# Kernel tuning notes

Hardware: AMD Instinct MI355X
Metric: run time of the kernel (lower is better)

The kernel has to match this reference:

```python
import jax, jax.numpy as jnp
import numpy as np

B, S, H = 1, 2048, 2048
E, I = 16, 1408
I_SHARED = 5632
TOP_K = 2


def setup_inputs() -> dict:
    key = jax.random.key(0)
    ks = jax.random.split(key, 8)
    scale = 0.02
    return {
        "hidden_states": jax.random.normal(ks[0], (B, S, H), dtype=jnp.float32),
        "router_w": jax.random.normal(ks[1], (H, E), dtype=jnp.float32) * scale,
        "expert_gate_up_w": jax.random.normal(ks[2], (E, H, 2 * I), dtype=jnp.float32) * scale,
        "expert_out_w": jax.random.normal(ks[3], (E, I, H), dtype=jnp.float32) * scale,
        "shared_ffw_gate_w": jax.random.normal(ks[4], (H, I_SHARED), dtype=jnp.float32) * scale,
        "shared_ffw_inter_w": jax.random.normal(ks[5], (H, I_SHARED), dtype=jnp.float32) * scale,
        "shared_ffw_out_w": jax.random.normal(ks[6], (I_SHARED, H), dtype=jnp.float32) * scale,
        "shared_gate_w": jax.random.normal(ks[7], (H, 1), dtype=jnp.float32) * scale,
        "top_k": TOP_K,
    }


def reference(hidden_states, router_w, expert_gate_up_w, expert_out_w,
              shared_ffw_gate_w, shared_ffw_inter_w, shared_ffw_out_w,
              shared_gate_w, top_k):
    b, s, h = hidden_states.shape
    e = router_w.shape[-1]
    x = hidden_states.reshape(-1, h)  # [T, H]

    # --- Router: softmax over experts, top-k, renormalize (norm_top_k_prob=True) ---
    router_logits = x @ router_w                        # [T, E]
    router_probs = jax.nn.softmax(router_logits, -1)
    top_p, top_i = jax.lax.top_k(router_probs, top_k)   # [T, K]
    top_p = top_p / jnp.sum(top_p, axis=-1, keepdims=True)
    # dense routing matrix [E, T] (matches one_hot-sum-transpose in source)
    one_hot = jax.nn.one_hot(top_i, e, dtype=top_p.dtype)  # [T, K, E]
    routing_full = jnp.sum(one_hot * top_p[..., None], axis=1).T  # [E, T]

    # --- Dense per-expert SwiGLU over ALL tokens (as in QwenMoeExperts) ---
    gate_up = jnp.einsum('th,ehm->etm', x, expert_gate_up_w)  # [E, T, 2I]
    gate, up = jnp.split(gate_up, 2, axis=-1)
    hidden = up * jax.nn.silu(gate)                           # [E, T, I]
    expert_out = jnp.einsum('eti,eih->eth', hidden, expert_out_w)  # [E, T, H]
    expert_contribution = jnp.einsum('eth,et->th', expert_out, routing_full)

    # --- Shared expert (SwiGLU MLP) with sigmoid gate ---
    sgate = jax.nn.silu(x @ shared_ffw_gate_w)
    sinter = x @ shared_ffw_inter_w
    shared_out = (sinter * sgate) @ shared_ffw_out_w          # [T, H]
    shared_out = shared_out * jax.nn.sigmoid(x @ shared_gate_w)

    out = (expert_contribution + shared_out).reshape(b, s, h)
    return out, router_logits
```

## Files before the change

### kernel.cpp

```cpp
#include <hip/hip_runtime.h>
#include <math.h>

typedef __attribute__((ext_vector_type(4))) float f32x4;
typedef __attribute__((ext_vector_type(2))) unsigned int u32x2;
typedef __attribute__((ext_vector_type(4))) unsigned int u32x4;
typedef __attribute__((ext_vector_type(8))) unsigned short u16x8;
typedef __attribute__((ext_vector_type(8))) __bf16 bf16x8;
typedef unsigned short ushort_t;

#define H_DIM 2048
#define T_TOK 2048
#define NEXP 16
#define I_DIM 1408
#define I2_DIM 2816
#define IS_DIM 5632
#define MAXROWS 8192

static __device__ __forceinline__ unsigned short f2bf(float f){
  union { float f; unsigned u; } v; v.f = f;
  unsigned r = v.u + 0x7FFFu + ((v.u >> 16) & 1u);
  return (unsigned short)(r >> 16);
}
static __device__ __forceinline__ float bf2f(unsigned short h){
  union { unsigned u; float f; } v; v.u = ((unsigned)h) << 16;
  return v.f;
}
static __device__ __forceinline__ float silu_f(float x){ return x / (1.f + __expf(-x)); }

static __device__ __forceinline__ void gld16(const ushort_t* g, ushort_t* l){
  __builtin_amdgcn_global_load_lds(
      (const __attribute__((address_space(1))) unsigned int*)g,
      (__attribute__((address_space(3))) unsigned int*)l, 16, 0, 0);
}

__global__ void cast_bf16_k(const float* __restrict__ in, ushort_t* __restrict__ out){
  long i = ((long)blockIdx.x * 256 + threadIdx.x) * 8;
  f32x4 a = *(const f32x4*)&in[i];
  f32x4 b = *(const f32x4*)&in[i + 4];
  union { ushort_t s[8]; u32x4 v; } pk;
  #pragma unroll
  for (int j = 0; j < 4; j++){ pk.s[j] = f2bf(a[j]); pk.s[j+4] = f2bf(b[j]); }
  *(u32x4*)&out[i] = pk.v;
}

__global__ void transpose_cast_k(const float* __restrict__ in, ushort_t* __restrict__ out,
                                 int K, int N){
  long zo = (long)blockIdx.z * K * N;
  in += zo; out += zo;
  __shared__ float tl[32][33];
  int n0 = blockIdx.x * 32, k0 = blockIdx.y * 32;
  int tid = threadIdx.x;
  int tx = tid & 31, ty = tid >> 5;
  #pragma unroll
  for (int j = 0; j < 4; j++)
    tl[ty + j*8][tx] = in[(long)(k0 + ty + j*8) * N + n0 + tx];
  __syncthreads();
  int nl = tid >> 3, kc = (tid & 7) * 4;
  unsigned w0 = (unsigned)f2bf(tl[kc+0][nl]) | ((unsigned)f2bf(tl[kc+1][nl]) << 16);
  unsigned w1 = (unsigned)f2bf(tl[kc+2][nl]) | ((unsigned)f2bf(tl[kc+3][nl]) << 16);
  u32x2 o; o[0] = w0; o[1] = w1;
  *(u32x2*)&out[(long)(n0 + nl) * K + k0 + kc] = o;
}

__global__ void router_k(const float* __restrict__ x, const float* __restrict__ rw,
                         const float* __restrict__ sgw, float* __restrict__ logits,
                         int* __restrict__ counts, int* __restrict__ lists,
                         float* __restrict__ probs, float* __restrict__ sgmul){
  int wid = threadIdx.x >> 6, lane = threadIdx.x & 63;
  int t = blockIdx.x * 4 + wid;
  const float* xr = x + (long)t * H_DIM;
  float acc[17];
  #pragma unroll
  for (int e = 0; e < 17; e++) acc[e] = 0.f;
  for (int h0 = lane * 4; h0 < H_DIM; h0 += 256){
    f32x4 xv = *(const f32x4*)&xr[h0];
    #pragma unroll
    for (int i = 0; i < 4; i++){
      float xs = xv[i];
      const float* wrow = rw + (long)(h0 + i) * NEXP;
      #pragma unroll
      for (int e = 0; e < 16; e++) acc[e] += xs * wrow[e];
      acc[16] += xs * sgw[h0 + i];
    }
  }
  #pragma unroll
  for (int e = 0; e < 17; e++)
    for (int off = 32; off >= 1; off >>= 1)
      acc[e] += __shfl_xor(acc[e], off);
  if (lane == 0){
    float* lo = logits + (long)t * NEXP;
    #pragma unroll
    for (int e = 0; e < 16; e++) lo[e] = acc[e];
    int e0 = 0;
    #pragma unroll
    for (int e = 1; e < 16; e++) if (acc[e] > acc[e0]) e0 = e;
    int e1 = (e0 == 0) ? 1 : 0;
    #pragma unroll
    for (int e = 0; e < 16; e++) if (e != e0 && acc[e] > acc[e1]) e1 = e;
    float d = acc[e1] - acc[e0];
    float ed = __expf(d);
    float p0 = 1.f / (1.f + ed);
    float p1 = ed / (1.f + ed);
    int pos0 = atomicAdd(&counts[e0], 1);
    lists[e0 * T_TOK + pos0] = t; probs[e0 * T_TOK + pos0] = p0;
    int pos1 = atomicAdd(&counts[e1], 1);
    lists[e1 * T_TOK + pos1] = t; probs[e1 * T_TOK + pos1] = p1;
    sgmul[t] = 1.f / (1.f + __expf(-acc[16]));
  }
}

__global__ void bases_k(const int* __restrict__ counts, int* __restrict__ bases){
  if (threadIdx.x == 0){
    int r = 0;
    for (int e = 0; e < NEXP; e++){ bases[e] = r; r += (counts[e] + 255) & ~255; }
  }
}

__global__ void swiglu_expert_k(const ushort_t* __restrict__ gu, ushort_t* __restrict__ hid){
  long qd = (long)blockIdx.x * 256 + threadIdx.x;
  long r = qd / (I_DIM / 8); int ic = (int)(qd % (I_DIM / 8)) * 8;
  const ushort_t* g = gu + r * I2_DIM + ic;
  u16x8 gv = *(const u16x8*)g;
  u16x8 uv = *(const u16x8*)(g + I_DIM);
  u16x8 ov;
  #pragma unroll
  for (int i = 0; i < 8; i++)
    ov[i] = f2bf(bf2f(uv[i]) * silu_f(bf2f(gv[i])));
  *(u16x8*)&hid[r * I_DIM + ic] = ov;
}

__global__ void swiglu_flat_k(ushort_t* __restrict__ sg, const ushort_t* __restrict__ si){
  long i = ((long)blockIdx.x * 256 + threadIdx.x) * 8;
  u16x8 g = *(const u16x8*)&sg[i];
  u16x8 s = *(const u16x8*)&si[i];
  u16x8 o;
  #pragma unroll
  for (int j = 0; j < 8; j++)
    o[j] = f2bf(bf2f(s[j]) * silu_f(bf2f(g[j])));
  *(u16x8*)&sg[i] = o;
}

template<int MODE>
__global__ __launch_bounds__(512, 2)
void gemm2_k(const ushort_t* __restrict__ A, const ushort_t* __restrict__ Bt,
             const ushort_t* __restrict__ Bt2, ushort_t* __restrict__ Cb,
             int K, int lda, int ldbt, int ldc, int mb,
             const int* __restrict__ counts, const int* __restrict__ bases,
             const int* __restrict__ lists, const float* __restrict__ probs,
             const float* __restrict__ svec, float* __restrict__ outp,
             long bstride){
  int z = blockIdx.z;
  int cnt = T_TOK;
  const ushort_t* Ab = A;
  const ushort_t* Bb = Bt;
  long rbase = 0;
  if constexpr (MODE == 0){ if (z){ Bb = Bt2; Cb += (long)T_TOK * ldc; } }
  if constexpr (MODE == 1){ cnt = counts[z]; rbase = bases[z]; Bb += (long)z * bstride; }
  if constexpr (MODE == 2){ cnt = counts[z]; Ab += (long)bases[z] * lda; Bb += (long)z * bstride; }

  int kb = K / gridDim.y;
  int kbase = blockIdx.y * kb;
  Ab += kbase;
  Bb += kbase;

  int nwg = gridDim.x;
  int wgo = blockIdx.x;
  int q = nwg >> 3, r = nwg & 7;
  int xcd = wgo & 7, idx = wgo >> 3;
  int wg = (xcd < r ? xcd * (q + 1) : r * (q + 1) + (xcd - r) * q) + idx;
  int m0 = (wg % mb) * 256;
  if (m0 >= cnt) return;
  int n0 = (wg / mb) * 256;

  extern __shared__ ushort_t lds[];

  int tid = threadIdx.x;
  int lane = tid & 63;
  int wv = tid >> 6;
  int wm = wv >> 2;
  int wn = wv & 3;

  int sg = ((lane & 7) ^ (lane >> 3)) * 8;
  long aoff[4], boff[4];
  #pragma unroll
  for (int i = 0; i < 4; i++){
    int mr = wv * 32 + i * 8 + (lane >> 3);
    int grow;
    if constexpr (MODE == 1){
      int j = m0 + mr; if (j >= cnt) j = cnt - 1;
      grow = lists[z * T_TOK + j];
    } else {
      grow = m0 + mr;
    }
    aoff[i] = (long)grow * lda + sg;
    boff[i] = (long)(n0 + mr) * ldbt + sg;
  }
  ushort_t* stA = lds + (size_t)(wv * 32) * 64;
  ushort_t* stB = lds + 16384 + (size_t)(wv * 32) * 64;

  f32x4 zero = {0.f, 0.f, 0.f, 0.f};
  f32x4 acc[8][4];
  #pragma unroll
  for (int i = 0; i < 8; i++)
    #pragma unroll
    for (int j = 0; j < 4; j++) acc[i][j] = zero;

  int nt = kb >> 6;
  #pragma unroll
  for (int i = 0; i < 4; i++){
    gld16(Ab + aoff[i], stA + i * 512);
    gld16(Bb + boff[i], stB + i * 512);
  }
  __syncthreads();

  int c = 0;
  for (int t = 0; t < nt; t++){
    if (t + 1 < nt){
      long ko = (long)(t + 1) * 64;
      int nb = (c ^ 1) * 32768;
      #pragma unroll
      for (int i = 0; i < 4; i++){
        gld16(Ab + aoff[i] + ko, stA + nb + i * 512);
        gld16(Bb + boff[i] + ko, stB + nb + i * 512);
      }
    }
    const ushort_t* tA = lds + c * 32768;
    const ushort_t* tB = tA + 16384;
    #pragma unroll
    for (int kk = 0; kk < 2; kk++){
      int cs = ((kk * 4 + (lane >> 4)) ^ (lane & 7)) * 8;
      bf16x8 af[8], bf[4];
      #pragma unroll
      for (int fm = 0; fm < 8; fm++)
        af[fm] = *(const bf16x8*)&tA[(wm*128 + fm*16 + (lane & 15)) * 64 + cs];
      #pragma unroll
      for (int fn = 0; fn < 4; fn++)
        bf[fn] = *(const bf16x8*)&tB[(wn*64 + fn*16 + (lane & 15)) * 64 + cs];
      #pragma unroll
      for (int fm = 0; fm < 8; fm++)
        #pragma unroll
        for (int fn = 0; fn < 4; fn++)
          acc[fm][fn] = __builtin_amdgcn_mfma_f32_16x16x32_bf16(af[fm], bf[fn], acc[fm][fn], 0, 0, 0);
    }
    if (t + 1 < nt) __syncthreads();
    c ^= 1;
  }

  int colb = n0 + wn * 64 + (lane & 15);
  int rowb = m0 + wm * 128 + (lane >> 4) * 4;
  #pragma unroll
  for (int fm = 0; fm < 8; fm++){
    #pragma unroll
    for (int fn = 0; fn < 4; fn++){
      f32x4 v = acc[fm][fn];
      int col = colb + fn * 16;
      #pragma unroll
      for (int rr = 0; rr < 4; rr++){
        int m = rowb + fm * 16 + rr;
        if constexpr (MODE == 0){
          Cb[(long)m * ldc + col] = f2bf(v[rr]);
        } else if constexpr (MODE == 1){
          if (m < cnt) Cb[(rbase + m) * (long)ldc + col] = f2bf(v[rr]);
        } else if constexpr (MODE == 2){
          if (m < cnt){
            int tok = lists[z * T_TOK + m];
            float pp = probs[z * T_TOK + m];
            atomicAdd(outp + (long)tok * ldc + col, pp * v[rr]);
          }
        } else {
          atomicAdd(outp + (long)m * ldc + col, svec[m] * v[rr]);
        }
      }
    }
  }
}

extern "C" void kernel_launch(void* const* d_in, const int* in_sizes, int n_in,
                              void* d_out, int out_size, void* d_ws, size_t ws_size,
                              hipStream_t stream){
  const float* x    = (const float*)d_in[0];
  const float* rw   = (const float*)d_in[1];
  const float* wgu  = (const float*)d_in[2];
  const float* wout = (const float*)d_in[3];
  const float* wsg  = (const float*)d_in[4];
  const float* wsi  = (const float*)d_in[5];
  const float* wso  = (const float*)d_in[6];
  const float* sgw  = (const float*)d_in[7];

  float* out = (float*)d_out;
  float* logits = out + (size_t)T_TOK * H_DIM;

  char* w = (char*)d_ws;
  auto alloc = [&](size_t b){ char* p = w; w += (b + 255) & ~(size_t)255; return p; };
  ushort_t* xb     = (ushort_t*)alloc((size_t)T_TOK * H_DIM * 2);
  ushort_t* wgu_t  = (ushort_t*)alloc((size_t)NEXP * I2_DIM * H_DIM * 2);
  ushort_t* wout_t = (ushort_t*)alloc((size_t)NEXP * H_DIM * I_DIM * 2);
  ushort_t* wsg_t  = (ushort_t*)alloc((size_t)IS_DIM * H_DIM * 2);
  ushort_t* wsi_t  = (ushort_t*)alloc((size_t)IS_DIM * H_DIM * 2);
  ushort_t* wso_t  = (ushort_t*)alloc((size_t)H_DIM * IS_DIM * 2);
  ushort_t* sgr    = (ushort_t*)alloc((size_t)2 * T_TOK * IS_DIM * 2);
  ushort_t* sir    = sgr + (size_t)T_TOK * IS_DIM;
  ushort_t* gu     = (ushort_t*)alloc((size_t)MAXROWS * I2_DIM * 2);
  ushort_t* hid    = (ushort_t*)alloc((size_t)MAXROWS * I_DIM * 2);
  int*   counts = (int*)alloc(64);
  int*   bases  = (int*)alloc(64);
  int*   lists  = (int*)alloc((size_t)NEXP * T_TOK * 4);
  float* probs  = (float*)alloc((size_t)NEXP * T_TOK * 4);
  float* sgmul  = (float*)alloc((size_t)T_TOK * 4);

  hipMemsetAsync(counts, 0, 64, stream);
  hipMemsetAsync(out, 0, (size_t)T_TOK * H_DIM * sizeof(float), stream);

  cast_bf16_k<<<2048, 256, 0, stream>>>(x, xb);
  transpose_cast_k<<<dim3(I2_DIM/32, H_DIM/32, NEXP), 256, 0, stream>>>(wgu, wgu_t, H_DIM, I2_DIM);
  transpose_cast_k<<<dim3(H_DIM/32, I_DIM/32, NEXP), 256, 0, stream>>>(wout, wout_t, I_DIM, H_DIM);
  transpose_cast_k<<<dim3(IS_DIM/32, H_DIM/32, 1), 256, 0, stream>>>(wsg, wsg_t, H_DIM, IS_DIM);
  transpose_cast_k<<<dim3(IS_DIM/32, H_DIM/32, 1), 256, 0, stream>>>(wsi, wsi_t, H_DIM, IS_DIM);
  transpose_cast_k<<<dim3(H_DIM/32, IS_DIM/32, 1), 256, 0, stream>>>(wso, wso_t, IS_DIM, H_DIM);

  router_k<<<512, 256, 0, stream>>>(x, rw, sgw, logits, counts, lists, probs, sgmul);
  bases_k<<<1, 64, 0, stream>>>(counts, bases);

  const size_t LDSB = 2 * 2 * 256 * 64 * sizeof(ushort_t);

  gemm2_k<0><<<dim3((T_TOK/256) * (IS_DIM/256), 1, 2), 512, LDSB, stream>>>(
      xb, wsg_t, wsi_t, sgr, H_DIM, H_DIM, H_DIM, IS_DIM, T_TOK/256,
      nullptr, nullptr, nullptr, nullptr, nullptr, nullptr, 0);
  swiglu_flat_k<<<(T_TOK * (IS_DIM/8)) / 256, 256, 0, stream>>>(sgr, sir);
  gemm2_k<3><<<dim3((T_TOK/256) * (H_DIM/256), 4, 1), 512, LDSB, stream>>>(
      sgr, wso_t, nullptr, nullptr, IS_DIM, IS_DIM, IS_DIM, H_DIM, T_TOK/256,
      nullptr, nullptr, nullptr, nullptr, sgmul, out, 0);

  gemm2_k<1><<<dim3((T_TOK/256) * (I2_DIM/256), 1, NEXP), 512, LDSB, stream>>>(
      xb, wgu_t, nullptr, gu, H_DIM, H_DIM, H_DIM, I2_DIM, T_TOK/256,
      counts, bases, lists, probs, nullptr, nullptr, (long)I2_DIM * H_DIM);
  swiglu_expert_k<<<((long)MAXROWS * (I_DIM/8)) / 256, 256, 0, stream>>>(gu, hid);
  gemm2_k<2><<<dim3((T_TOK/256) * (H_DIM/256), 1, NEXP), 512, LDSB, stream>>>(
      hid, wout_t, nullptr, nullptr, I_DIM, I_DIM, I_DIM, H_DIM, T_TOK/256,
      counts, bases, lists, probs, nullptr, out, (long)I_DIM * H_DIM);

  (void)in_sizes; (void)n_in; (void)out_size; (void)ws_size;
}
```

Before: 878.1 us.

## Widen transpose-cast tiles and reorder GEMM prefetch after LDS fragment reads

The weight transpose-cast kernel now uses 64x64 tiles with 16-byte vector loads and 16-byte packed bf16 stores, replacing 32x32 tiles with scalar accesses. This cuts the number of memory transactions in the weight conversion pass, at the cost of a larger LDS tile. In the GEMM main loop, each wave reads all LDS fragments for both k-substeps first, then issues the next tile's global-to-LDS prefetch, then runs the MFMAs, with a sched_barrier and a sync every iteration. This aims to overlap global loads with the MFMAs, but it holds more fragment registers live, which could lower occupancy.

Result: slower. 924.2 us (+5.3%).

```diff
diff --git a/kernel.cpp b/kernel.cpp
--- a/kernel.cpp
+++ b/kernel.cpp
@@ -47,19 +47,29 @@
                                  int K, int N){
   long zo = (long)blockIdx.z * K * N;
   in += zo; out += zo;
-  __shared__ float tl[32][33];
-  int n0 = blockIdx.x * 32, k0 = blockIdx.y * 32;
+  __shared__ float tl[64][65];
+  int n0 = blockIdx.x * 64, k0 = blockIdx.y * 64;
   int tid = threadIdx.x;
-  int tx = tid & 31, ty = tid >> 5;
-  #pragma unroll
-  for (int j = 0; j < 4; j++)
-    tl[ty + j*8][tx] = in[(long)(k0 + ty + j*8) * N + n0 + tx];
+  int lr = tid >> 2;
+  int lv = (tid & 3) * 4;
+  #pragma unroll
+  for (int j = 0; j < 4; j++){
+    int col = lv + j * 16;
+    f32x4 v = *(const f32x4*)&in[(long)(k0 + lr) * N + n0 + col];
+    tl[lr][col + 0] = v[0]; tl[lr][col + 1] = v[1];
+    tl[lr][col + 2] = v[2]; tl[lr][col + 3] = v[3];
+  }
   __syncthreads();
-  int nl = tid >> 3, kc = (tid & 7) * 4;
-  unsigned w0 = (unsigned)f2bf(tl[kc+0][nl]) | ((unsigned)f2bf(tl[kc+1][nl]) << 16);
-  unsigned w1 = (unsigned)f2bf(tl[kc+2][nl]) | ((unsigned)f2bf(tl[kc+3][nl]) << 16);
-  u32x2 o; o[0] = w0; o[1] = w1;
-  *(u32x2*)&out[(long)(n0 + nl) * K + k0 + kc] = o;
+  int nl = tid >> 3;
+  int kc = (tid & 7) * 8;
+  #pragma unroll
+  for (int it = 0; it < 2; it++){
+    int n = nl + it * 32;
+    union { ushort_t s[8]; u32x4 v; } pk;
+    #pragma unroll
+    for (int j = 0; j < 8; j++) pk.s[j] = f2bf(tl[kc + j][n]);
+    *(u32x4*)&out[(long)(n0 + n) * K + k0 + kc] = pk.v;
+  }
 }
 
 __global__ void router_k(const float* __restrict__ x, const float* __restrict__ rw,
@@ -181,22 +191,35 @@
   int wn = wv & 3;
 
   int sg = ((lane & 7) ^ (lane >> 3)) * 8;
-  long aoff[4], boff[4];
-  #pragma unroll
-  for (int i = 0; i < 4; i++){
-    int mr = wv * 32 + i * 8 + (lane >> 3);
-    int grow;
+  long aoff0, boff0;
+  long aoffg[4];
+  {
+    int r0 = wv * 32 + (lane >> 3);
     if constexpr (MODE == 1){
-      int j = m0 + mr; if (j >= cnt) j = cnt - 1;
-      grow = lists[z * T_TOK + j];
+      #pragma unroll
+      for (int i = 0; i < 4; i++){
+        int j = m0 + r0 + i * 8; if (j >= cnt) j = cnt - 1;
+        aoffg[i] = (long)lists[z * T_TOK + j] * lda + sg;
+      }
     } else {
-      grow = m0 + mr;
-    }
-    aoff[i] = (long)grow * lda + sg;
-    boff[i] = (long)(n0 + mr) * ldbt + sg;
-  }
-  ushort_t* stA = lds + (size_t)(wv * 32) * 64;
-  ushort_t* stB = lds + 16384 + (size_t)(wv * 32) * 64;
+      aoff0 = (long)(m0 + r0) * lda + sg;
+    }
+    boff0 = (long)(n0 + r0) * ldbt + sg;
+  }
+
+  auto stage = [&](long ko, int buf){
+    ushort_t* dA = lds + buf * 32768 + wv * 32 * 64;
+    ushort_t* dB = dA + 16384;
+    #pragma unroll
+    for (int i = 0; i < 4; i++){
+      long ao;
+      if constexpr (MODE == 1) ao = aoffg[i]; else ao = aoff0 + (long)(i * 8) * lda;
+      gld16(Ab + ao + ko, dA + i * 512);
+    }
+    #pragma unroll
+    for (int i = 0; i < 4; i++)
+      gld16(Bb + boff0 + (long)(i * 8) * ldbt + ko, dB + i * 512);
+  };
 
   f32x4 zero = {0.f, 0.f, 0.f, 0.f};
   f32x4 acc[8][4];
@@ -206,44 +229,34 @@
     for (int j = 0; j < 4; j++) acc[i][j] = zero;
 
   int nt = kb >> 6;
-  #pragma unroll
-  for (int i = 0; i < 4; i++){
-    gld16(Ab + aoff[i], stA + i * 512);
-    gld16(Bb + boff[i], stB + i * 512);
-  }
+  stage(0, 0);
   __syncthreads();
 
-  int c = 0;
   for (int t = 0; t < nt; t++){
-    if (t + 1 < nt){
-      long ko = (long)(t + 1) * 64;
-      int nb = (c ^ 1) * 32768;
-      #pragma unroll
-      for (int i = 0; i < 4; i++){
-        gld16(Ab + aoff[i] + ko, stA + nb + i * 512);
-        gld16(Bb + boff[i] + ko, stB + nb + i * 512);
-      }
-    }
+    int c = t & 1;
     const ushort_t* tA = lds + c * 32768;
     const ushort_t* tB = tA + 16384;
+    bf16x8 af[2][8], bf[2][4];
     #pragma unroll
     for (int kk = 0; kk < 2; kk++){
       int cs = ((kk * 4 + (lane >> 4)) ^ (lane & 7)) * 8;
-      bf16x8 af[8], bf[4];
       #pragma unroll
       for (int fm = 0; fm < 8; fm++)
-        af[fm] = *(const bf16x8*)&tA[(wm*128 + fm*16 + (lane & 15)) * 64 + cs];
+        af[kk][fm] = *(const bf16x8*)&tA[(wm*128 + fm*16 + (lane & 15)) * 64 + cs];
       #pragma unroll
       for (int fn = 0; fn < 4; fn++)
-        bf[fn] = *(const bf16x8*)&tB[(wn*64 + fn*16 + (lane & 15)) * 64 + cs];
+        bf[kk][fn] = *(const bf16x8*)&tB[(wn*64 + fn*16 + (lane & 15)) * 64 + cs];
+    }
+    __builtin_amdgcn_sched_barrier(0);
+    if (t + 1 < nt) stage((long)(t + 1) * 64, c ^ 1);
+    #pragma unroll
+    for (int kk = 0; kk < 2; kk++)
       #pragma unroll
       for (int fm = 0; fm < 8; fm++)
         #pragma unroll
         for (int fn = 0; fn < 4; fn++)
-          acc[fm][fn] = __builtin_amdgcn_mfma_f32_16x16x32_bf16(af[fm], bf[fn], acc[fm][fn], 0, 0, 0);
-    }
-    if (t + 1 < nt) __syncthreads();
-    c ^= 1;
+          acc[fm][fn] = __builtin_amdgcn_mfma_f32_16x16x32_bf16(af[kk][fm], bf[kk][fn], acc[fm][fn], 0, 0, 0);
+    __syncthreads();
   }
 
   int colb = n0 + wn * 64 + (lane & 15);
@@ -312,11 +325,11 @@
   hipMemsetAsync(out, 0, (size_t)T_TOK * H_DIM * sizeof(float), stream);
 
   cast_bf16_k<<<2048, 256, 0, stream>>>(x, xb);
-  transpose_cast_k<<<dim3(I2_DIM/32, H_DIM/32, NEXP), 256, 0, stream>>>(wgu, wgu_t, H_DIM, I2_DIM);
-  transpose_cast_k<<<dim3(H_DIM/32, I_DIM/32, NEXP), 256, 0, stream>>>(wout, wout_t, I_DIM, H_DIM);
-  transpose_cast_k<<<dim3(IS_DIM/32, H_DIM/32, 1), 256, 0, stream>>>(wsg, wsg_t, H_DIM, IS_DIM);
-  transpose_cast_k<<<dim3(IS_DIM/32, H_DIM/32, 1), 256, 0, stream>>>(wsi, wsi_t, H_DIM, IS_DIM);
-  transpose_cast_k<<<dim3(H_DIM/32, IS_DIM/32, 1), 256, 0, stream>>>(wso, wso_t, IS_DIM, H_DIM);
+  transpose_cast_k<<<dim3(I2_DIM/64, H_DIM/64, NEXP), 256, 0, stream>>>(wgu, wgu_t, H_DIM, I2_DIM);
+  transpose_cast_k<<<dim3(H_DIM/64, I_DIM/64, NEXP), 256, 0, stream>>>(wout, wout_t, I_DIM, H_DIM);
+  transpose_cast_k<<<dim3(IS_DIM/64, H_DIM/64, 1), 256, 0, stream>>>(wsg, wsg_t, H_DIM, IS_DIM);
+  transpose_cast_k<<<dim3(IS_DIM/64, H_DIM/64, 1), 256, 0, stream>>>(wsi, wsi_t, H_DIM, IS_DIM);
+  transpose_cast_k<<<dim3(H_DIM/64, IS_DIM/64, 1), 256, 0, stream>>>(wso, wso_t, IS_DIM, H_DIM);
 
   router_k<<<512, 256, 0, stream>>>(x, rw, sgw, logits, counts, lists, probs, sgmul);
   bases_k<<<1, 64, 0, stream>>>(counts, bases);
```
